# Optimization experiments

Measured on AMD Instinct MI355X. Metric: run time of the kernel, lower is better.

## Reference

```python
import jax, jax.numpy as jnp
import numpy as np

B, S, D, H = 64, 2048, 512, 512


def setup_inputs() -> dict:
    key = jax.random.key(0)
    ks = jax.random.split(key, 8)
    inp = jax.random.normal(ks[0], (B, D), dtype=jnp.float32)
    context = jax.random.normal(ks[1], (B, S, D), dtype=jnp.float32)
    mask = jax.random.randint(ks[2], (B, S), 0, 2).astype(jnp.int32)
    alpha_mask = jax.random.uniform(ks[3], (B, S), dtype=jnp.float32)
    sd = 1.0 / np.sqrt(D)
    W_in = jax.random.uniform(ks[4], (H, D), minval=-sd, maxval=sd, dtype=jnp.float32)
    b_in = jnp.zeros((H,), dtype=jnp.float32)
    W_ctx = jax.random.uniform(ks[5], (H, D), minval=-sd, maxval=sd, dtype=jnp.float32)  # Conv1d k=1 == pointwise linear
    b_ctx = jnp.zeros((H,), dtype=jnp.float32)
    V = jax.random.uniform(ks[6], (H,), minval=-1.0, maxval=1.0, dtype=jnp.float32)
    return {"input": inp, "context": context, "alpha_mask": alpha_mask,
            "W_in": W_in, "b_in": b_in, "W_ctx": W_ctx, "b_ctx": b_ctx, "V": V,
            "mask": mask}


def reference(input, context, alpha_mask, W_in, b_in, W_ctx, b_ctx, V, mask):
    seq_len = context.shape[1]
    # input_linear: [B, H]
    inp = input @ W_in.T + b_in
    # context_linear (Conv1d kernel=1 over permuted context): [B, H, S]
    ctx = jnp.einsum('hd,bsd->bhs', W_ctx, context) + b_ctx[None, :, None]
    # additive attention energies: V . tanh(inp + ctx) -> [B, S]
    att = jnp.einsum('h,bhs->bs', V, jnp.tanh(inp[:, :, None] + ctx))
    # mask branching (faithful to the torch data-dependent branch, jit-safe):
    # if any(mask) and count(mask) == S: att[mask] = -inf; else: att = att * alpha_mask
    mb = mask != 0
    n_true = jnp.sum(mb)
    take_inf_branch = (n_true > 0) & (n_true == seq_len)
    att = jnp.where(take_inf_branch,
                    jnp.where(mb, -jnp.inf, att),
                    att * alpha_mask)
    alpha = jax.nn.softmax(att, axis=-1)  # [B, S]
    # context vector: bmm(ctx [B,H,S], alpha [B,S,1]) -> [B, H]
    hidden_state = jnp.einsum('bhs,bs->bh', ctx, alpha)
    return hidden_state, alpha
```

## Files before the change

kernel.cpp:

```cpp
#include <hip/hip_runtime.h>
#include <math.h>

#define B 64
#define S 2048
#define D 512
#define H 512

typedef _Float16 f16x8 __attribute__((ext_vector_type(8)));
typedef _Float16 f16x4 __attribute__((ext_vector_type(4)));
typedef __fp16 fp16x2 __attribute__((ext_vector_type(2)));
typedef float f32x4 __attribute__((ext_vector_type(4)));

#define LDA 40
#define WSC 128

#define WS_CBAR_OFF (512 * 1024)
#define WS_CNT_OFF  (640 * 1024)

__global__ __launch_bounds__(256) void k_pack_wc(
        const float* __restrict__ Wc, _Float16* __restrict__ wsB) {
    const int slot = blockIdx.x * 256 + threadIdx.x;
    const int kt   = slot >> 11;
    const int rem  = slot & 2047;
    const int hg   = rem >> 6;
    const int lane = rem & 63;
    const int h  = hg * 16 + (lane & 15);
    const int k0 = kt * 32 + (lane >> 4) * 8;
    const float* src = Wc + (size_t)h * D + k0;
    float4 f0 = *(const float4*)src;
    float4 f1 = *(const float4*)(src + 4);
    f16x8 v;
    v[0] = (_Float16)f0.x; v[1] = (_Float16)f0.y;
    v[2] = (_Float16)f0.z; v[3] = (_Float16)f0.w;
    v[4] = (_Float16)f1.x; v[5] = (_Float16)f1.y;
    v[6] = (_Float16)f1.z; v[7] = (_Float16)f1.w;
    *(f16x8*)(wsB + (size_t)slot * 8) = v;
}

__global__ __launch_bounds__(256) void k_mask_count(
        const int* __restrict__ mask, int* __restrict__ cnt) {
    const int base = blockIdx.x * 256 + threadIdx.x;
    int local = 0;
    for (int i = base; i < B * S; i += 256 * 64) local += (mask[i] != 0) ? 1 : 0;
    #pragma unroll
    for (int off = 32; off; off >>= 1) local += __shfl_down(local, off, 64);
    if ((threadIdx.x & 63) == 0 && local) atomicAdd(cnt, local);
}

__global__ __launch_bounds__(256) void k_input_linear(
        const float* __restrict__ input,
        const float* __restrict__ W_in,
        const float* __restrict__ b_in,
        float* __restrict__ out_inp) {
    const int b = blockIdx.x;
    const int tid = threadIdx.x;
    __shared__ float xrow[D];
    for (int d = tid; d < D; d += 256) xrow[d] = input[(size_t)b * D + d];
    __syncthreads();
    for (int h = tid; h < H; h += 256) {
        const float* w = W_in + (size_t)h * D;
        float acc = 0.f;
        #pragma unroll 4
        for (int d = 0; d < D; d += 4) {
            float4 wv = *(const float4*)(w + d);
            acc += wv.x * xrow[d] + wv.y * xrow[d + 1] + wv.z * xrow[d + 2] + wv.w * xrow[d + 3];
        }
        out_inp[(size_t)b * H + h] = acc + b_in[h];
    }
}

__global__ __launch_bounds__(512, 4) void k_energy(
        const float* __restrict__ ctx,
        const _Float16* __restrict__ WcP,
        const float* __restrict__ bc,
        const float* __restrict__ inp,
        const float* __restrict__ V,
        float* __restrict__ att) {
    __shared__ alignas(16) _Float16 Alds[2][64 * LDA];
    __shared__ float red[8][64];

    const int tid = threadIdx.x;
    const int b  = blockIdx.x >> 5;
    const int s0 = (blockIdx.x & 31) << 6;

    const int arow = tid >> 3;
    const int akq  = tid & 7;
    const int lane = tid & 63;
    const int w    = tid >> 6;
    const int lrow = lane & 15;
    const int kblk = lane >> 4;

    f32x4 acc[4][4] = {};

    const float* ctx_src = ctx + ((size_t)b * S + s0 + arow) * D + akq * 4;
    const _Float16* Abase = &Alds[0][lrow * LDA + kblk * 8];
    const _Float16* Bbase = WcP + ((size_t)(w * 4) * 64 + lane) * 8;

    {
        float4 f = *(const float4*)ctx_src;
        union { fp16x2 h2[2]; f16x4 v; } u;
        u.h2[0] = __builtin_amdgcn_cvt_pkrtz(f.x, f.y);
        u.h2[1] = __builtin_amdgcn_cvt_pkrtz(f.z, f.w);
        *(f16x4*)&Alds[0][arow * LDA + akq * 4] = u.v;
    }
    __syncthreads();

    #pragma unroll 1
    for (int kt = 0; kt < 16; ++kt) {
        const int cur = kt & 1;

        float4 nf;
        if (kt < 15) nf = *(const float4*)(ctx_src + (kt + 1) * 32);

        f16x8 bfr[4];
        #pragma unroll
        for (int n = 0; n < 4; ++n)
            bfr[n] = *(const f16x8*)(Bbase + ((size_t)kt * 2048 + n * 64) * 8);

        f16x8 afr[4];
        #pragma unroll
        for (int m = 0; m < 4; ++m)
            afr[m] = *(const f16x8*)(Abase + cur * (64 * LDA) + m * 16 * LDA);

        #pragma unroll
        for (int m = 0; m < 4; ++m)
            #pragma unroll
            for (int n = 0; n < 4; ++n)
                acc[m][n] = __builtin_amdgcn_mfma_f32_16x16x32_f16(afr[m], bfr[n], acc[m][n], 0, 0, 0);

        if (kt < 15) {
            union { fp16x2 h2[2]; f16x4 v; } u;
            u.h2[0] = __builtin_amdgcn_cvt_pkrtz(nf.x, nf.y);
            u.h2[1] = __builtin_amdgcn_cvt_pkrtz(nf.z, nf.w);
            *(f16x4*)&Alds[cur ^ 1][arow * LDA + akq * 4] = u.v;
        }
        __syncthreads();
    }

    float ps[4][4] = {};
    #pragma unroll
    for (int n = 0; n < 4; ++n) {
        const int h = w * 64 + n * 16 + lrow;
        const float ib = inp[(size_t)b * H + h] + bc[h];
        const float v = V[h];
        #pragma unroll
        for (int m = 0; m < 4; ++m)
            #pragma unroll
            for (int r = 0; r < 4; ++r) {
                const float x = acc[m][n][r] + ib;
                const float t = 1.f - 2.f / (1.f + __expf(2.f * x));
                ps[m][r] += v * t;
            }
    }
    #pragma unroll
    for (int off = 1; off < 16; off <<= 1)
        #pragma unroll
        for (int m = 0; m < 4; ++m)
            #pragma unroll
            for (int r = 0; r < 4; ++r)
                ps[m][r] += __shfl_xor(ps[m][r], off, 64);
    if (lrow == 0) {
        #pragma unroll
        for (int m = 0; m < 4; ++m)
            #pragma unroll
            for (int r = 0; r < 4; ++r)
                red[w][m * 16 + kblk * 4 + r] = ps[m][r];
    }
    __syncthreads();
    if (tid < 64) {
        float sum = 0.f;
        #pragma unroll
        for (int i = 0; i < 8; ++i) sum += red[i][tid];
        att[(size_t)b * S + s0 + tid] = sum;
    }
}

__global__ __launch_bounds__(256) void k_softmax(
        const int* __restrict__ mask,
        const float* __restrict__ amask,
        const int* __restrict__ cnt,
        float* __restrict__ att) {
    const int b = blockIdx.x;
    const int tid = threadIdx.x;
    __shared__ float sh[S];
    __shared__ float fredm[4];
    __shared__ float freds[4];

    const int n_true = *cnt;
    const bool inf_branch = (n_true > 0) && (n_true == S);

    const float NEG_INF = -__builtin_inff();
    for (int s = tid; s < S; s += 256) {
        const float raw = att[(size_t)b * S + s];
        float v;
        if (inf_branch)
            v = mask[(size_t)b * S + s] ? NEG_INF : raw;
        else
            v = raw * amask[(size_t)b * S + s];
        sh[s] = v;
    }
    __syncthreads();

    float mx = NEG_INF;
    for (int s = tid; s < S; s += 256) mx = fmaxf(mx, sh[s]);
    #pragma unroll
    for (int off = 32; off; off >>= 1) mx = fmaxf(mx, __shfl_down(mx, off, 64));
    if ((tid & 63) == 0) fredm[tid >> 6] = mx;
    __syncthreads();
    mx = fmaxf(fmaxf(fredm[0], fredm[1]), fmaxf(fredm[2], fredm[3]));

    float lsum = 0.f;
    for (int s = tid; s < S; s += 256) {
        const float e = expf(sh[s] - mx);
        sh[s] = e;
        lsum += e;
    }
    #pragma unroll
    for (int off = 32; off; off >>= 1) lsum += __shfl_down(lsum, off, 64);
    if ((tid & 63) == 0) freds[tid >> 6] = lsum;
    __syncthreads();
    const float total = freds[0] + freds[1] + freds[2] + freds[3];
    const float rinv = 1.f / total;

    for (int s = tid; s < S; s += 256)
        att[(size_t)b * S + s] = sh[s] * rinv;
}

__global__ __launch_bounds__(256) void k_wsum(
        const float* __restrict__ ctx,
        const float* __restrict__ alpha,
        float* __restrict__ cbar) {
    const int chunk = blockIdx.x & 15;
    const int b = blockIdx.x >> 4;
    const int s0 = chunk * WSC;
    const int tid = threadIdx.x;
    __shared__ float al[WSC];
    if (tid < WSC) al[tid] = alpha[(size_t)b * S + s0 + tid];
    __syncthreads();

    const int half = tid >> 7;
    const int dq = (tid & 127) * 4;
    const float* base = ctx + ((size_t)b * S + s0 + half) * D + dq;
    float4 acc = {0.f, 0.f, 0.f, 0.f};
    #pragma unroll 4
    for (int i = 0; i < WSC / 2; ++i) {
        float4 v = *(const float4*)(base + (size_t)i * 2 * D);
        const float a = al[i * 2 + half];
        acc.x += a * v.x; acc.y += a * v.y; acc.z += a * v.z; acc.w += a * v.w;
    }
    float* dst = cbar + (size_t)b * D + dq;
    atomicAdd(dst + 0, acc.x);
    atomicAdd(dst + 1, acc.y);
    atomicAdd(dst + 2, acc.z);
    atomicAdd(dst + 3, acc.w);
}

__global__ __launch_bounds__(256) void k_out(
        const float* __restrict__ cbar,
        const float* __restrict__ Wc,
        const float* __restrict__ bc,
        float* __restrict__ hidden) {
    const int b = blockIdx.x;
    const int tid = threadIdx.x;
    __shared__ float cb[D];
    for (int d = tid; d < D; d += 256) cb[d] = cbar[(size_t)b * D + d];
    __syncthreads();
    for (int h = tid; h < H; h += 256) {
        const float* w = Wc + (size_t)h * D;
        float acc = 0.f;
        #pragma unroll 4
        for (int d = 0; d < D; d += 4) {
            float4 wv = *(const float4*)(w + d);
            acc += wv.x * cb[d] + wv.y * cb[d + 1] + wv.z * cb[d + 2] + wv.w * cb[d + 3];
        }
        hidden[(size_t)b * H + h] = acc + bc[h];
    }
}

extern "C" void kernel_launch(void* const* d_in, const int* in_sizes, int n_in,
                              void* d_out, int out_size, void* d_ws, size_t ws_size,
                              hipStream_t stream) {
    const float* input = (const float*)d_in[0];
    const float* ctx   = (const float*)d_in[1];
    const float* amask = (const float*)d_in[2];
    const float* W_in  = (const float*)d_in[3];
    const float* b_in  = (const float*)d_in[4];
    const float* W_ctx = (const float*)d_in[5];
    const float* b_ctx = (const float*)d_in[6];
    const float* V     = (const float*)d_in[7];
    const int*   mask  = (const int*)d_in[8];

    float* out = (float*)d_out;
    float* hidden = out;
    float* alpha  = out + B * H;

    _Float16* wsB  = (_Float16*)d_ws;
    float*    cbar = (float*)((char*)d_ws + WS_CBAR_OFF);
    int*      cnt  = (int*)((char*)d_ws + WS_CNT_OFF);

    k_pack_wc<<<dim3(128), dim3(256), 0, stream>>>(W_ctx, wsB);
    (void)hipMemsetAsync(cnt, 0, sizeof(int), stream);
    k_mask_count<<<dim3(64), dim3(256), 0, stream>>>(mask, cnt);

    k_input_linear<<<dim3(B), dim3(256), 0, stream>>>(input, W_in, b_in, hidden);

    k_energy<<<dim3(B * S / 64), dim3(512), 0, stream>>>(
        ctx, wsB, b_ctx, hidden, V, alpha);

    k_softmax<<<dim3(B), dim3(256), 0, stream>>>(mask, amask, cnt, alpha);

    (void)hipMemsetAsync(cbar, 0, (size_t)B * D * sizeof(float), stream);
    k_wsum<<<dim3(16 * B), dim3(256), 0, stream>>>(ctx, alpha, cbar);

    k_out<<<dim3(B), dim3(256), 0, stream>>>(cbar, W_ctx, b_ctx, hidden);
}
```

Before: 245.4 us.

## Load energy A-tiles directly from global, replace atomics with partial sums

The energy kernel no longer stages the context tile through double-buffered LDS with per-iteration barriers. Each lane now loads its own fp32 A fragments straight from global memory and converts them to fp16 in registers. The weighted-sum kernel writes per-chunk partial results that k_out reduces, instead of using atomics onto a zeroed buffer. Both memset launches are removed, and the counter reset is folded into the pack kernel. The risk is that direct global loads are less coalesced and have no prefetch, so memory latency in the MFMA loop may be exposed.

```diff
diff --git a/kernel.cpp b/kernel.cpp
--- a/kernel.cpp
+++ b/kernel.cpp
@@ -7,18 +7,18 @@
 #define H 512
 
 typedef _Float16 f16x8 __attribute__((ext_vector_type(8)));
-typedef _Float16 f16x4 __attribute__((ext_vector_type(4)));
 typedef __fp16 fp16x2 __attribute__((ext_vector_type(2)));
 typedef float f32x4 __attribute__((ext_vector_type(4)));
 
-#define LDA 40
 #define WSC 128
 
-#define WS_CBAR_OFF (512 * 1024)
-#define WS_CNT_OFF  (640 * 1024)
+#define WS_PART_OFF (512 * 1024)
+#define WS_CNT_OFF  (512 * 1024 + 2 * 1024 * 1024)
 
 __global__ __launch_bounds__(256) void k_pack_wc(
-        const float* __restrict__ Wc, _Float16* __restrict__ wsB) {
+        const float* __restrict__ Wc, _Float16* __restrict__ wsB,
+        int* __restrict__ cnt) {
+    if (blockIdx.x == 0 && threadIdx.x == 0) *cnt = 0;
     const int slot = blockIdx.x * 256 + threadIdx.x;
     const int kt   = slot >> 11;
     const int rem  = slot & 2047;
@@ -76,15 +76,12 @@
         const float* __restrict__ inp,
         const float* __restrict__ V,
         float* __restrict__ att) {
-    __shared__ alignas(16) _Float16 Alds[2][64 * LDA];
     __shared__ float red[8][64];
 
     const int tid = threadIdx.x;
     const int b  = blockIdx.x >> 5;
     const int s0 = (blockIdx.x & 31) << 6;
 
-    const int arow = tid >> 3;
-    const int akq  = tid & 7;
     const int lane = tid & 63;
     const int w    = tid >> 6;
     const int lrow = lane & 15;
@@ -92,26 +89,11 @@
 
     f32x4 acc[4][4] = {};
 
-    const float* ctx_src = ctx + ((size_t)b * S + s0 + arow) * D + akq * 4;
-    const _Float16* Abase = &Alds[0][lrow * LDA + kblk * 8];
+    const float* Abase = ctx + ((size_t)b * S + s0 + lrow) * D + kblk * 8;
     const _Float16* Bbase = WcP + ((size_t)(w * 4) * 64 + lane) * 8;
-
-    {
-        float4 f = *(const float4*)ctx_src;
-        union { fp16x2 h2[2]; f16x4 v; } u;
-        u.h2[0] = __builtin_amdgcn_cvt_pkrtz(f.x, f.y);
-        u.h2[1] = __builtin_amdgcn_cvt_pkrtz(f.z, f.w);
-        *(f16x4*)&Alds[0][arow * LDA + akq * 4] = u.v;
-    }
-    __syncthreads();
 
     #pragma unroll 1
     for (int kt = 0; kt < 16; ++kt) {
-        const int cur = kt & 1;
-
-        float4 nf;
-        if (kt < 15) nf = *(const float4*)(ctx_src + (kt + 1) * 32);
-
         f16x8 bfr[4];
         #pragma unroll
         for (int n = 0; n < 4; ++n)
@@ -119,22 +101,23 @@
 
         f16x8 afr[4];
         #pragma unroll
-        for (int m = 0; m < 4; ++m)
-            afr[m] = *(const f16x8*)(Abase + cur * (64 * LDA) + m * 16 * LDA);
+        for (int m = 0; m < 4; ++m) {
+            const float* src = Abase + (size_t)(m * 16) * D + kt * 32;
+            float4 f0 = *(const float4*)src;
+            float4 f1 = *(const float4*)(src + 4);
+            union { fp16x2 h2[4]; f16x8 v; } u;
+            u.h2[0] = __builtin_amdgcn_cvt_pkrtz(f0.x, f0.y);
+            u.h2[1] = __builtin_amdgcn_cvt_pkrtz(f0.z, f0.w);
+            u.h2[2] = __builtin_amdgcn_cvt_pkrtz(f1.x, f1.y);
+            u.h2[3] = __builtin_amdgcn_cvt_pkrtz(f1.z, f1.w);
+            afr[m] = u.v;
+        }
 
         #pragma unroll
         for (int m = 0; m < 4; ++m)
             #pragma unroll
             for (int n = 0; n < 4; ++n)
                 acc[m][n] = __builtin_amdgcn_mfma_f32_16x16x32_f16(afr[m], bfr[n], acc[m][n], 0, 0, 0);
-
-        if (kt < 15) {
-            union { fp16x2 h2[2]; f16x4 v; } u;
-            u.h2[0] = __builtin_amdgcn_cvt_pkrtz(nf.x, nf.y);
-            u.h2[1] = __builtin_amdgcn_cvt_pkrtz(nf.z, nf.w);
-            *(f16x4*)&Alds[cur ^ 1][arow * LDA + akq * 4] = u.v;
-        }
-        __syncthreads();
     }
 
     float ps[4][4] = {};
@@ -229,7 +212,7 @@
 __global__ __launch_bounds__(256) void k_wsum(
         const float* __restrict__ ctx,
         const float* __restrict__ alpha,
-        float* __restrict__ cbar) {
+        float* __restrict__ part) {
     const int chunk = blockIdx.x & 15;
     const int b = blockIdx.x >> 4;
     const int s0 = chunk * WSC;
@@ -248,22 +231,33 @@
         const float a = al[i * 2 + half];
         acc.x += a * v.x; acc.y += a * v.y; acc.z += a * v.z; acc.w += a * v.w;
     }
-    float* dst = cbar + (size_t)b * D + dq;
-    atomicAdd(dst + 0, acc.x);
-    atomicAdd(dst + 1, acc.y);
-    atomicAdd(dst + 2, acc.z);
-    atomicAdd(dst + 3, acc.w);
+    __shared__ float cb[2][D];
+    *(float4*)&cb[half][dq] = acc;
+    __syncthreads();
+    if (tid < 128) {
+        const int d = tid * 4;
+        float4 p0 = *(const float4*)&cb[0][d];
+        float4 p1 = *(const float4*)&cb[1][d];
+        float4 o = {p0.x + p1.x, p0.y + p1.y, p0.z + p1.z, p0.w + p1.w};
+        *(float4*)(part + ((size_t)chunk * B + b) * D + d) = o;
+    }
 }
 
 __global__ __launch_bounds__(256) void k_out(
-        const float* __restrict__ cbar,
+        const float* __restrict__ part,
         const float* __restrict__ Wc,
         const float* __restrict__ bc,
         float* __restrict__ hidden) {
     const int b = blockIdx.x;
     const int tid = threadIdx.x;
     __shared__ float cb[D];
-    for (int d = tid; d < D; d += 256) cb[d] = cbar[(size_t)b * D + d];
+    for (int d = tid; d < D; d += 256) {
+        float s = 0.f;
+        #pragma unroll
+        for (int c = 0; c < 16; ++c)
+            s += part[((size_t)c * B + b) * D + d];
+        cb[d] = s;
+    }
     __syncthreads();
     for (int h = tid; h < H; h += 256) {
         const float* w = Wc + (size_t)h * D;
@@ -295,11 +289,10 @@
     float* alpha  = out + B * H;
 
     _Float16* wsB  = (_Float16*)d_ws;
-    float*    cbar = (float*)((char*)d_ws + WS_CBAR_OFF);
+    float*    part = (float*)((char*)d_ws + WS_PART_OFF);
     int*      cnt  = (int*)((char*)d_ws + WS_CNT_OFF);
 
-    k_pack_wc<<<dim3(128), dim3(256), 0, stream>>>(W_ctx, wsB);
-    (void)hipMemsetAsync(cnt, 0, sizeof(int), stream);
+    k_pack_wc<<<dim3(128), dim3(256), 0, stream>>>(W_ctx, wsB, cnt);
     k_mask_count<<<dim3(64), dim3(256), 0, stream>>>(mask, cnt);
 
     k_input_linear<<<dim3(B), dim3(256), 0, stream>>>(input, W_in, b_in, hidden);
@@ -309,8 +302,7 @@
 
     k_softmax<<<dim3(B), dim3(256), 0, stream>>>(mask, amask, cnt, alpha);
 
-    (void)hipMemsetAsync(cbar, 0, (size_t)B * D * sizeof(float), stream);
-    k_wsum<<<dim3(16 * B), dim3(256), 0, stream>>>(ctx, alpha, cbar);
-
-    k_out<<<dim3(B), dim3(256), 0, stream>>>(cbar, W_ctx, b_ctx, hidden);
-}
+    k_wsum<<<dim3(16 * B), dim3(256), 0, stream>>>(ctx, alpha, part);
+
+    k_out<<<dim3(B), dim3(256), 0, stream>>>(part, W_ctx, b_ctx, hidden);
+}
```

Result: slower. 410.4 us (+67.3%).
